# Performance work log

Measured on AMD Instinct MI355X. Metric: run time of the kernel, lower is better.

## Reference

```python
import jax, jax.numpy as jnp
import numpy as np

D_MODEL = 1024
NUM_HEADS = 16
HEAD_DIM = D_MODEL // NUM_HEADS  # used only for score scaling, as in the torch code


def setup_inputs() -> dict:
    key = jax.random.key(0)
    ks = jax.random.split(key, 8)
    B, S, D = 4, 2048, D_MODEL
    w_scale = 1.0 / np.sqrt(D)
    return {
        "x": jax.random.normal(ks[0], (B, S, D), dtype=jnp.float32),
        "Wq": jax.random.normal(ks[1], (D, D), dtype=jnp.float32) * w_scale,
        "bq": jnp.zeros((D,), dtype=jnp.float32),
        "Wk": jax.random.normal(ks[2], (D, D), dtype=jnp.float32) * w_scale,
        "bk": jnp.zeros((D,), dtype=jnp.float32),
        "Wv": jax.random.normal(ks[3], (D, D), dtype=jnp.float32) * w_scale,
        "bv": jnp.zeros((D,), dtype=jnp.float32),
        "temperature_scale": jnp.ones((1,), dtype=jnp.float32),
    }


def reference(x, Wq, bq, Wk, bk, Wv, bv, temperature_scale):
    # q, k, v: (B, S, D) -- no head split in the original module
    q = x @ Wq + bq
    k = x @ Wk + bk
    v = x @ Wv + bv
    scale = jnp.asarray(HEAD_DIM, x.dtype) ** 0.5
    # scores: (B, S, S)
    scores = jnp.einsum("bqd,bkd->bqk", q, k) / scale / temperature_scale[0]
    probs = jax.nn.softmax(scores, axis=-1)
    # per-row attention entropy (B, S, 1)
    entropy = -jnp.sum(probs * jnp.log(probs + 1e-8), axis=-1, keepdims=True)
    attention_output = jnp.einsum("bqk,bkd->bqd", probs, v)
    return attention_output, entropy.mean()
```

## Files before the change

kernel.cpp:

```cpp
#include <hip/hip_runtime.h>
#include <hip/hip_bf16.h>
#include <cstdint>
#include <cstddef>


typedef __attribute__((ext_vector_type(8))) short short8;
typedef __attribute__((ext_vector_type(4))) short short4v;
typedef __attribute__((ext_vector_type(4))) float f32x4;

#define GLOBAL_AS __attribute__((address_space(1)))
#define LDS_AS __attribute__((address_space(3)))

__device__ __forceinline__ void async_load16(const void* g, void* lds) {
  __builtin_amdgcn_global_load_lds((GLOBAL_AS void*)g, (LDS_AS void*)lds, 16, 0, 0);
}

__device__ __forceinline__ short f2bf_s(float x) {
  __hip_bfloat16 h = __float2bfloat16(x);
  return *reinterpret_cast<short*>(&h);
}

template <int MODE>
__device__ __forceinline__
void gemm256_body(const __hip_bfloat16* __restrict__ A,
                  const __hip_bfloat16* __restrict__ Bt,
                  void* __restrict__ Cout,
                  const float* __restrict__ bias,
                  int K, int lda, int ldb, int ldc,
                  __hip_bfloat16* __restrict__ sA,
                  __hip_bfloat16* __restrict__ sB,
                  int m0, int n0,
                  const float* __restrict__ aux,
                  float* __restrict__ stats) {
  const int tid  = threadIdx.x;
  const int lane = tid & 63;
  const int wid  = tid >> 6;
  const int wm   = (wid >> 2) * 128;
  const int wn   = (wid & 3) * 64;
  const int quad = lane >> 4;
  const int rc   = lane & 15;
  const int rc7  = rc & 7;
  const int wnr  = wn & 64;

  f32x4 acc[8][4] = {};

  const int r0   = tid >> 3;
  const int scol = ((tid & 7) ^ (r0 & 7)) * 8;
  const __hip_bfloat16* Ag = A  + (size_t)(m0 + r0) * lda + scol;
  const __hip_bfloat16* Bg = Bt + (size_t)(n0 + r0) * ldb + scol;

  const int NT = K >> 6;

  auto stA = [&](int buf, int half, int kofs) {
    const __hip_bfloat16* s = Ag + (size_t)(half * 128) * lda + kofs;
    __hip_bfloat16* d = sA + (size_t)buf * 16384 + (size_t)half * 8192 + tid * 8;
    async_load16(s, d);
    async_load16(s + (size_t)64 * lda, d + 4096);
  };
  auto stB = [&](int buf, int half, int kofs) {
    const __hip_bfloat16* s = Bg + (size_t)(half * 128) * ldb + kofs;
    __hip_bfloat16* d = sB + (size_t)buf * 16384 + (size_t)half * 8192 + tid * 8;
    async_load16(s, d);
    async_load16(s + (size_t)64 * ldb, d + 4096);
  };

  const __hip_bfloat16* sAh0 = sA + (size_t)(wm >> 7) * 8192;
  const __hip_bfloat16* sBh0 = sB + (size_t)(wn >> 7) * 8192;

  {
    const int k1 = (NT > 1 ? 1 : 0) * 64;
    stA(0, 0, 0); stA(0, 1, 0); stB(0, 0, 0); stB(0, 1, 0);
    stB(1, 0, k1); stB(1, 1, k1); stA(1, 0, k1);
  }
  asm volatile("s_waitcnt vmcnt(6)" ::: "memory");
  __builtin_amdgcn_s_barrier();

  for (int t = 0; t < NT; ++t) {
    const int buf = t & 1;
    const __hip_bfloat16* sAc = sAh0 + buf * 16384;
    const __hip_bfloat16* sBc = sBh0 + buf * 16384;
    const int k1 = ((t + 1 < NT) ? t + 1 : NT - 1) * 64;
    const int k2 = ((t + 2 < NT) ? t + 2 : NT - 1) * 64;

    short8 af[2][4], bfr[2][4], ah[2][4];

#pragma unroll
    for (int kk = 0; kk < 2; ++kk) {
      const int gs = (kk * 4 + quad) ^ rc7;
#pragma unroll
      for (int i = 0; i < 4; ++i)
        af[kk][i] = *(const short8*)&sAc[(i * 16 + rc) * 64 + gs * 8];
#pragma unroll
      for (int j = 0; j < 4; ++j)
        bfr[kk][j] = *(const short8*)&sBc[(wnr + j * 16 + rc) * 64 + gs * 8];
    }
    stA(buf ^ 1, 1, k1);
    __builtin_amdgcn_s_barrier();
    __builtin_amdgcn_s_setprio(1);
#pragma unroll
    for (int mi = 0; mi < 4; ++mi)
#pragma unroll
      for (int ni = 0; ni < 2; ++ni)
#pragma unroll
        for (int kk = 0; kk < 2; ++kk)
          acc[mi][ni] = __builtin_amdgcn_mfma_f32_16x16x32_bf16(
              af[kk][mi], bfr[kk][ni], acc[mi][ni], 0, 0, 0);
    __builtin_amdgcn_s_setprio(0);
    __builtin_amdgcn_s_barrier();

    __builtin_amdgcn_s_setprio(1);
#pragma unroll
    for (int mi = 0; mi < 4; ++mi)
#pragma unroll
      for (int ni = 2; ni < 4; ++ni)
#pragma unroll
        for (int kk = 0; kk < 2; ++kk)
          acc[mi][ni] = __builtin_amdgcn_mfma_f32_16x16x32_bf16(
              af[kk][mi], bfr[kk][ni], acc[mi][ni], 0, 0, 0);
    __builtin_amdgcn_s_setprio(0);
    __builtin_amdgcn_s_barrier();

#pragma unroll
    for (int kk = 0; kk < 2; ++kk) {
      const int gs = (kk * 4 + quad) ^ rc7;
#pragma unroll
      for (int i = 0; i < 4; ++i)
        ah[kk][i] = *(const short8*)&sAc[((i + 4) * 16 + rc) * 64 + gs * 8];
    }
    stB(buf, 0, k2);
    __builtin_amdgcn_s_barrier();
    __builtin_amdgcn_s_setprio(1);
#pragma unroll
    for (int mi = 0; mi < 4; ++mi)
#pragma unroll
      for (int ni = 0; ni < 2; ++ni)
#pragma unroll
        for (int kk = 0; kk < 2; ++kk)
          acc[4 + mi][ni] = __builtin_amdgcn_mfma_f32_16x16x32_bf16(
              ah[kk][mi], bfr[kk][ni], acc[4 + mi][ni], 0, 0, 0);
    __builtin_amdgcn_s_setprio(0);
    __builtin_amdgcn_s_barrier();

    stB(buf, 1, k2);
    stA(buf, 0, k2);
    __builtin_amdgcn_s_barrier();
    __builtin_amdgcn_s_setprio(1);
#pragma unroll
    for (int mi = 0; mi < 4; ++mi)
#pragma unroll
      for (int ni = 2; ni < 4; ++ni)
#pragma unroll
        for (int kk = 0; kk < 2; ++kk)
          acc[4 + mi][ni] = __builtin_amdgcn_mfma_f32_16x16x32_bf16(
              ah[kk][mi], bfr[kk][ni], acc[4 + mi][ni], 0, 0, 0);
    __builtin_amdgcn_s_setprio(0);
    asm volatile("s_waitcnt vmcnt(6)" ::: "memory");
    __builtin_amdgcn_s_barrier();
  }
  asm volatile("s_waitcnt vmcnt(0)" ::: "memory");

  if (MODE == 3) {
    const int chunk = (n0 + wn) >> 6;
#pragma unroll
    for (int mi = 0; mi < 8; ++mi) {
      float l_acc[4] = {}, w_acc[4] = {};
#pragma unroll
      for (int ni = 0; ni < 4; ++ni)
#pragma unroll
        for (int r = 0; r < 4; ++r) {
          const float xv = acc[mi][ni][r];
          const float e = __expf(xv);
          acc[mi][ni][r] = e;
          l_acc[r] += e;
          w_acc[r] += e * xv;
        }
#pragma unroll
      for (int r = 0; r < 4; ++r) {
        float l = l_acc[r], w = w_acc[r];
#pragma unroll
        for (int off = 1; off < 16; off <<= 1) {
          l += __shfl_xor(l, off);
          w += __shfl_xor(w, off);
        }
        if (rc == 0) {
          const int row = m0 + wm + mi * 16 + quad * 4 + r;
          *(float2*)&stats[((size_t)row * 32 + chunk) * 2] = make_float2(l, w);
        }
      }
#pragma unroll
      for (int ni = 0; ni < 4; ++ni) {
        const int col = n0 + wn + ni * 16 + rc;
#pragma unroll
        for (int r = 0; r < 4; ++r) {
          const int row = m0 + wm + mi * 16 + quad * 4 + r;
          ((__hip_bfloat16*)Cout)[(size_t)row * ldc + col] =
              __float2bfloat16(acc[mi][ni][r]);
        }
      }
    }
  } else {
    const float qsc = (MODE == 1 && aux) ? 1.0f / (8.0f * aux[0]) : 1.0f;
#pragma unroll
    for (int mi = 0; mi < 8; ++mi) {
#pragma unroll
      for (int ni = 0; ni < 4; ++ni) {
        const int col = n0 + wn + ni * 16 + rc;
        const float badd = bias[col];
        if (MODE == 2) {
          const int rowb = m0 + wm + mi * 16 + quad * 4;
          short4v o;
#pragma unroll
          for (int r = 0; r < 4; ++r) o[r] = f2bf_s(acc[mi][ni][r] + badd);
          const size_t idx = (size_t)(rowb >> 11) * (1024u * 2048u) +
                             (size_t)col * 2048u + (size_t)(rowb & 2047);
          *(short4v*)((short*)Cout + idx) = o;
        } else {
#pragma unroll
          for (int r = 0; r < 4; ++r) {
            const int row = m0 + wm + mi * 16 + quad * 4 + r;
            ((__hip_bfloat16*)Cout)[(size_t)row * ldc + col] =
                __float2bfloat16((acc[mi][ni][r] + badd) * qsc);
          }
        }
      }
    }
  }
}

__global__ __launch_bounds__(512, 2)
void qkv_fused256(const __hip_bfloat16* __restrict__ xb,
                  const __hip_bfloat16* __restrict__ Wt,
                  __hip_bfloat16* __restrict__ qb, __hip_bfloat16* __restrict__ kb,
                  __hip_bfloat16* __restrict__ vt,
                  const float* __restrict__ bq, const float* __restrict__ bk,
                  const float* __restrict__ bv, const float* __restrict__ tptr) {
  extern __shared__ __align__(16) __hip_bfloat16 smem[];
  __hip_bfloat16* sA = smem;
  __hip_bfloat16* sB = smem + 32768;
  const int lin = blockIdx.x;
  const int G  = (lin & 7) * 48 + (lin >> 3);
  const int mt = G / 12, nt = G % 12;
  const int m0  = mt * 256;
  const int n0g = nt * 256;
  const int z   = n0g >> 10;
  const int n0  = n0g & 1023;
  const __hip_bfloat16* B = Wt + (size_t)z * 1024 * 1024;
  if (z == 0)
    gemm256_body<1>(xb, B, qb, bq, 1024, 1024, 1024, 1024, sA, sB, m0, n0, tptr, nullptr);
  else if (z == 1)
    gemm256_body<1>(xb, B, kb, bk, 1024, 1024, 1024, 1024, sA, sB, m0, n0, nullptr, nullptr);
  else
    gemm256_body<2>(xb, B, vt, bv, 1024, 1024, 1024, 0, sA, sB, m0, n0, nullptr, nullptr);
}

__global__ __launch_bounds__(512, 2)
void scores256(const __hip_bfloat16* __restrict__ qb,
               const __hip_bfloat16* __restrict__ kb,
               __hip_bfloat16* __restrict__ Pt,
               float* __restrict__ stats) {
  extern __shared__ __align__(16) __hip_bfloat16 smem[];
  __hip_bfloat16* sA = smem;
  __hip_bfloat16* sB = smem + 32768;
  const int lin = blockIdx.x;
  const int G = (lin & 7) * 32 + (lin >> 3);
  const int z = G >> 6;
  const int r = G & 63;
  const int y = r >> 3, x = r & 7;
  gemm256_body<3>(qb + (size_t)z * 2048 * 1024, kb + (size_t)z * 2048 * 1024,
                  Pt + (size_t)z * 2048 * 2048, nullptr, 1024, 1024, 1024, 2048,
                  sA, sB, y * 256, x * 256, nullptr, stats + (size_t)z * 2048 * 64);
}

template <int MODE>
__device__ __forceinline__
void gemm_body(const __hip_bfloat16* __restrict__ A,
               const __hip_bfloat16* __restrict__ Bt,
               void* __restrict__ Cout,
               const float* __restrict__ bias,
               int K, int lda, int ldb, int ldc,
               __hip_bfloat16* __restrict__ sA,
               __hip_bfloat16* __restrict__ sB,
               int m0, int n0,
               const float* __restrict__ aux,
               float* __restrict__ stats) {
  const int tid  = threadIdx.x;
  const int lane = tid & 63;
  const int wid  = tid >> 6;
  const int wm = (wid >> 1) * 64;
  const int wn = (wid & 1) * 64;
  const int quad = lane >> 4;
  const int rc   = lane & 15;

  f32x4 acc[4][4] = {};

  const int srow = tid >> 3;
  const int scol = ((tid & 7) ^ ((tid >> 3) & 7)) * 8;
  const __hip_bfloat16* Ag = A  + (size_t)(m0 + srow) * lda + scol;
  const __hip_bfloat16* Bg = Bt + (size_t)(n0 + srow) * ldb + scol;

  for (int k0 = 0; k0 < K; k0 += 64) {
#pragma unroll
    for (int p = 0; p < 4; ++p) {
      async_load16(Ag + k0 + (size_t)(32 * p) * lda, &sA[(wid * 64 + 256 * p) * 8]);
      async_load16(Bg + k0 + (size_t)(32 * p) * ldb, &sB[(wid * 64 + 256 * p) * 8]);
    }
    __syncthreads();

#pragma unroll
    for (int kk = 0; kk < 2; ++kk) {
      const int xo = ((kk * 4 + quad) ^ (rc & 7)) * 8;
      short8 af[4], bf[4];
#pragma unroll
      for (int i = 0; i < 4; ++i)
        af[i] = *(const short8*)&sA[(wm + i * 16 + rc) * 64 + xo];
#pragma unroll
      for (int i = 0; i < 4; ++i)
        bf[i] = *(const short8*)&sB[(wn + i * 16 + rc) * 64 + xo];

#pragma unroll
      for (int mi = 0; mi < 4; ++mi)
#pragma unroll
        for (int ni = 0; ni < 4; ++ni)
          acc[mi][ni] = __builtin_amdgcn_mfma_f32_16x16x32_bf16(
              af[mi], bf[ni], acc[mi][ni], 0, 0, 0);
    }
    __syncthreads();
  }

  if (MODE == 4) {
#pragma unroll
    for (int mi = 0; mi < 4; ++mi) {
      float sc[4];
#pragma unroll
      for (int r = 0; r < 4; ++r)
        sc[r] = aux[m0 + wm + mi * 16 + quad * 4 + r];
#pragma unroll
      for (int ni = 0; ni < 4; ++ni) {
        const int col = n0 + wn + ni * 16 + rc;
#pragma unroll
        for (int r = 0; r < 4; ++r) {
          const int row = m0 + wm + mi * 16 + quad * 4 + r;
          ((float*)Cout)[(size_t)row * ldc + col] = acc[mi][ni][r] * sc[r];
        }
      }
    }
  }
}

__global__ __launch_bounds__(256)
void pv_swz(const __hip_bfloat16* __restrict__ Pt,
            const __hip_bfloat16* __restrict__ vt,
            float* __restrict__ out,
            const float* __restrict__ inv_l) {
  __shared__ __align__(16) __hip_bfloat16 sA[128 * 64];
  __shared__ __align__(16) __hip_bfloat16 sB[128 * 64];
  const int lin = blockIdx.x;
  const int j = lin & 7, t = lin >> 3;
  const int w = t & 3;
  const int G = j + 8 * (t >> 2);
  const size_t z = G >> 5;
  const int r = G & 31;
  const int y = (r >> 2) * 2 + (w >> 1);
  const int x = (r & 3) * 2 + (w & 1);
  gemm_body<4>(Pt + z * 2048 * 2048, vt + z * 1024 * 2048,
               out + z * 2048 * 1024, nullptr, 2048, 2048, 2048, 1024,
               sA, sB, y * 128, x * 128, inv_l + z * 2048, nullptr);
}

__global__ __launch_bounds__(256)
void cast_f32_to_bf16(const float* __restrict__ src,
                      __hip_bfloat16* __restrict__ dst, int n) {
  const int i = (blockIdx.x * 256 + threadIdx.x) * 8;
  if (i >= n) return;
  const float4 a = *(const float4*)(src + i);
  const float4 b = *(const float4*)(src + i + 4);
  short8 o;
  o[0] = f2bf_s(a.x); o[1] = f2bf_s(a.y); o[2] = f2bf_s(a.z); o[3] = f2bf_s(a.w);
  o[4] = f2bf_s(b.x); o[5] = f2bf_s(b.y); o[6] = f2bf_s(b.z); o[7] = f2bf_s(b.w);
  *(short8*)((short*)dst + i) = o;
}

__global__ __launch_bounds__(256)
void transpose_cast_3w(const float* __restrict__ Wq, const float* __restrict__ Wk,
                       const float* __restrict__ Wv,
                       __hip_bfloat16* __restrict__ Wt) {
  __shared__ float tile[64][65];
  const int z = blockIdx.z;
  const float* src = (z == 0) ? Wq : (z == 1) ? Wk : Wv;
  __hip_bfloat16* dst = Wt + (size_t)z * 1024 * 1024;
  const int c0 = blockIdx.x * 64;
  const int r0 = blockIdx.y * 64;
  const int lane = threadIdx.x & 63;
  const int grp  = threadIdx.x >> 6;
#pragma unroll
  for (int i = 0; i < 16; ++i) {
    const int r = grp * 16 + i;
    tile[r][lane] = src[(size_t)(r0 + r) * 1024 + c0 + lane];
  }
  __syncthreads();
#pragma unroll
  for (int i = 0; i < 16; ++i) {
    const int r = grp * 16 + i;
    dst[(size_t)(c0 + r) * 1024 + r0 + lane] = __float2bfloat16(tile[lane][r]);
  }
}

__global__ __launch_bounds__(256)
void stats_reduce(const float* __restrict__ stats,
                  float* __restrict__ inv_l, float* __restrict__ Hrow) {
  const int row = blockIdx.x * 256 + threadIdx.x;
  const float* sp = stats + (size_t)row * 64;
  float l = 0.f, w = 0.f;
#pragma unroll
  for (int j = 0; j < 16; ++j) {
    const float4 a = *(const float4*)(sp + j * 4);
    l += a.x + a.z;
    w += a.y + a.w;
  }
  const float il = 1.0f / l;
  inv_l[row] = il;
  Hrow[row] = __logf(l) - w * il;
}

__global__ __launch_bounds__(256)
void reduce_entropy(const float* __restrict__ Hrow, float* __restrict__ out) {
  const int tid  = threadIdx.x;
  const int lane = tid & 63;
  const int wid  = tid >> 6;
  float s = 0.f;
#pragma unroll
  for (int j = 0; j < 8; ++j) {
    const float4 a = *(const float4*)(Hrow + j * 1024 + tid * 4);
    s += a.x + a.y + a.z + a.w;
  }
#pragma unroll
  for (int off = 1; off < 64; off <<= 1) s += __shfl_xor(s, off);
  __shared__ float red[4];
  if (lane == 0) red[wid] = s;
  __syncthreads();
  if (tid == 0)
    out[0] = (red[0] + red[1] + red[2] + red[3]) * (1.0f / 8192.0f);
}

extern "C" void kernel_launch(void* const* d_in, const int* in_sizes, int n_in,
                              void* d_out, int out_size, void* d_ws, size_t ws_size,
                              hipStream_t stream) {
  const float* x    = (const float*)d_in[0];
  const float* Wq   = (const float*)d_in[1];
  const float* bq   = (const float*)d_in[2];
  const float* Wk   = (const float*)d_in[3];
  const float* bk   = (const float*)d_in[4];
  const float* Wv   = (const float*)d_in[5];
  const float* bv   = (const float*)d_in[6];
  const float* temp = (const float*)d_in[7];
  float* out = (float*)d_out;
  char* ws = (char*)d_ws;

  __hip_bfloat16* qb    = (__hip_bfloat16*)(ws + 0);
  __hip_bfloat16* kb    = (__hip_bfloat16*)(ws + 16777216);
  __hip_bfloat16* vt    = (__hip_bfloat16*)(ws + 33554432);
  __hip_bfloat16* xb    = (__hip_bfloat16*)(ws + 50331648);
  __hip_bfloat16* Wt    = (__hip_bfloat16*)(ws + 67108864);
  __hip_bfloat16* Pt    = (__hip_bfloat16*)(ws + 73400320);
  float*          stats = (float*)(ws + 106954752);
  float*          inv_l = (float*)(ws + 109051904);
  float*          Hrow  = (float*)(ws + 109084672);

  static bool attr_done = false;
  if (!attr_done) {
    hipFuncSetAttribute((const void*)qkv_fused256,
                        hipFuncAttributeMaxDynamicSharedMemorySize, 131072);
    hipFuncSetAttribute((const void*)scores256,
                        hipFuncAttributeMaxDynamicSharedMemorySize, 131072);
    attr_done = true;
  }

  cast_f32_to_bf16<<<4096, 256, 0, stream>>>(x, xb, 8388608);
  transpose_cast_3w<<<dim3(16, 16, 3), 256, 0, stream>>>(Wq, Wk, Wv, Wt);

  qkv_fused256<<<384, 512, 131072, stream>>>(xb, Wt, qb, kb, vt, bq, bk, bv, temp);

  scores256<<<256, 512, 131072, stream>>>(qb, kb, Pt, stats);
  stats_reduce<<<32, 256, 0, stream>>>(stats, inv_l, Hrow);
  pv_swz<<<512, 256, 0, stream>>>(Pt, vt, out, inv_l);

  reduce_entropy<<<1, 256, 0, stream>>>(Hrow, out + 8388608);
}
```

Measured before the change: 256.3 us.

## Restructure GEMM main loop to prefetch next-tile fragments across phases

```diff
diff --git a/kernel.cpp b/kernel.cpp
--- a/kernel.cpp
+++ b/kernel.cpp
@@ -64,37 +64,44 @@
     async_load16(s + (size_t)64 * ldb, d + 4096);
   };
 
-  const __hip_bfloat16* sAh0 = sA + (size_t)(wm >> 7) * 8192;
-  const __hip_bfloat16* sBh0 = sB + (size_t)(wn >> 7) * 8192;
+  const __hip_bfloat16* sAh = sA + (size_t)(wm >> 7) * 8192;
+  const __hip_bfloat16* sBh = sB + (size_t)(wn >> 7) * 8192;
+
+  short8 af[2][4], ah[2][4], blo[2][2], bhi[2][2];
 
   {
-    const int k1 = (NT > 1 ? 1 : 0) * 64;
-    stA(0, 0, 0); stA(0, 1, 0); stB(0, 0, 0); stB(0, 1, 0);
-    stB(1, 0, k1); stB(1, 1, k1); stA(1, 0, k1);
-  }
-  asm volatile("s_waitcnt vmcnt(6)" ::: "memory");
+    const int k1 = (NT > 1) ? 64 : 0;
+    stA(0, 0, 0);  stA(0, 1, 0);  stB(0, 0, 0);  stB(0, 1, 0);
+    stA(1, 0, k1); stA(1, 1, k1); stB(1, 0, k1); stB(1, 1, k1);
+  }
+  asm volatile("s_waitcnt vmcnt(8)" ::: "memory");
   __builtin_amdgcn_s_barrier();
+#pragma unroll
+  for (int kk = 0; kk < 2; ++kk) {
+    const int gs = ((kk * 4 + quad) ^ rc7) * 8;
+#pragma unroll
+    for (int i = 0; i < 4; ++i)
+      af[kk][i] = *(const short8*)&sAh[(i * 16 + rc) * 64 + gs];
+#pragma unroll
+    for (int j = 0; j < 2; ++j)
+      blo[kk][j] = *(const short8*)&sBh[(wnr + j * 16 + rc) * 64 + gs];
+  }
 
   for (int t = 0; t < NT; ++t) {
     const int buf = t & 1;
-    const __hip_bfloat16* sAc = sAh0 + buf * 16384;
-    const __hip_bfloat16* sBc = sBh0 + buf * 16384;
-    const int k1 = ((t + 1 < NT) ? t + 1 : NT - 1) * 64;
+    const __hip_bfloat16* sAc = sAh + buf * 16384;
+    const __hip_bfloat16* sBc = sBh + buf * 16384;
+    const __hip_bfloat16* sAn = sAh + (buf ^ 1) * 16384;
+    const __hip_bfloat16* sBn = sBh + (buf ^ 1) * 16384;
     const int k2 = ((t + 2 < NT) ? t + 2 : NT - 1) * 64;
 
-    short8 af[2][4], bfr[2][4], ah[2][4];
-
 #pragma unroll
     for (int kk = 0; kk < 2; ++kk) {
-      const int gs = (kk * 4 + quad) ^ rc7;
+      const int gs = ((kk * 4 + quad) ^ rc7) * 8;
 #pragma unroll
       for (int i = 0; i < 4; ++i)
-        af[kk][i] = *(const short8*)&sAc[(i * 16 + rc) * 64 + gs * 8];
-#pragma unroll
-      for (int j = 0; j < 4; ++j)
-        bfr[kk][j] = *(const short8*)&sBc[(wnr + j * 16 + rc) * 64 + gs * 8];
-    }
-    stA(buf ^ 1, 1, k1);
+        ah[kk][i] = *(const short8*)&sAc[((i + 4) * 16 + rc) * 64 + gs];
+    }
     __builtin_amdgcn_s_barrier();
     __builtin_amdgcn_s_setprio(1);
 #pragma unroll
@@ -104,30 +111,18 @@
 #pragma unroll
         for (int kk = 0; kk < 2; ++kk)
           acc[mi][ni] = __builtin_amdgcn_mfma_f32_16x16x32_bf16(
-              af[kk][mi], bfr[kk][ni], acc[mi][ni], 0, 0, 0);
+              af[kk][mi], blo[kk][ni], acc[mi][ni], 0, 0, 0);
     __builtin_amdgcn_s_setprio(0);
     __builtin_amdgcn_s_barrier();
 
-    __builtin_amdgcn_s_setprio(1);
-#pragma unroll
-    for (int mi = 0; mi < 4; ++mi)
-#pragma unroll
-      for (int ni = 2; ni < 4; ++ni)
-#pragma unroll
-        for (int kk = 0; kk < 2; ++kk)
-          acc[mi][ni] = __builtin_amdgcn_mfma_f32_16x16x32_bf16(
-              af[kk][mi], bfr[kk][ni], acc[mi][ni], 0, 0, 0);
-    __builtin_amdgcn_s_setprio(0);
-    __builtin_amdgcn_s_barrier();
-
+    stA(buf, 0, k2);
 #pragma unroll
     for (int kk = 0; kk < 2; ++kk) {
-      const int gs = (kk * 4 + quad) ^ rc7;
-#pragma unroll
-      for (int i = 0; i < 4; ++i)
-        ah[kk][i] = *(const short8*)&sAc[((i + 4) * 16 + rc) * 64 + gs * 8];
-    }
-    stB(buf, 0, k2);
+      const int gs = ((kk * 4 + quad) ^ rc7) * 8;
+#pragma unroll
+      for (int j = 0; j < 2; ++j)
+        bhi[kk][j] = *(const short8*)&sBc[(wnr + (j + 2) * 16 + rc) * 64 + gs];
+    }
     __builtin_amdgcn_s_barrier();
     __builtin_amdgcn_s_setprio(1);
 #pragma unroll
@@ -137,24 +132,52 @@
 #pragma unroll
         for (int kk = 0; kk < 2; ++kk)
           acc[4 + mi][ni] = __builtin_amdgcn_mfma_f32_16x16x32_bf16(
-              ah[kk][mi], bfr[kk][ni], acc[4 + mi][ni], 0, 0, 0);
+              ah[kk][mi], blo[kk][ni], acc[4 + mi][ni], 0, 0, 0);
     __builtin_amdgcn_s_setprio(0);
     __builtin_amdgcn_s_barrier();
 
+    asm volatile("s_waitcnt vmcnt(2)" ::: "memory");
+    stA(buf, 1, k2);
+    stB(buf, 0, k2);
+#pragma unroll
+    for (int kk = 0; kk < 2; ++kk) {
+      const int gs = ((kk * 4 + quad) ^ rc7) * 8;
+#pragma unroll
+      for (int j = 0; j < 2; ++j)
+        blo[kk][j] = *(const short8*)&sBn[(wnr + j * 16 + rc) * 64 + gs];
+    }
+    __builtin_amdgcn_s_barrier();
+    __builtin_amdgcn_s_setprio(1);
+#pragma unroll
+    for (int mi = 0; mi < 4; ++mi)
+#pragma unroll
+      for (int nj = 0; nj < 2; ++nj)
+#pragma unroll
+        for (int kk = 0; kk < 2; ++kk)
+          acc[mi][2 + nj] = __builtin_amdgcn_mfma_f32_16x16x32_bf16(
+              af[kk][mi], bhi[kk][nj], acc[mi][2 + nj], 0, 0, 0);
+    __builtin_amdgcn_s_setprio(0);
+    __builtin_amdgcn_s_barrier();
+
     stB(buf, 1, k2);
-    stA(buf, 0, k2);
+#pragma unroll
+    for (int kk = 0; kk < 2; ++kk) {
+      const int gs = ((kk * 4 + quad) ^ rc7) * 8;
+#pragma unroll
+      for (int i = 0; i < 4; ++i)
+        af[kk][i] = *(const short8*)&sAn[(i * 16 + rc) * 64 + gs];
+    }
     __builtin_amdgcn_s_barrier();
     __builtin_amdgcn_s_setprio(1);
 #pragma unroll
     for (int mi = 0; mi < 4; ++mi)
 #pragma unroll
-      for (int ni = 2; ni < 4; ++ni)
+      for (int nj = 0; nj < 2; ++nj)
 #pragma unroll
         for (int kk = 0; kk < 2; ++kk)
-          acc[4 + mi][ni] = __builtin_amdgcn_mfma_f32_16x16x32_bf16(
-              ah[kk][mi], bfr[kk][ni], acc[4 + mi][ni], 0, 0, 0);
+          acc[4 + mi][2 + nj] = __builtin_amdgcn_mfma_f32_16x16x32_bf16(
+              ah[kk][mi], bhi[kk][nj], acc[4 + mi][2 + nj], 0, 0, 0);
     __builtin_amdgcn_s_setprio(0);
-    asm volatile("s_waitcnt vmcnt(6)" ::: "memory");
     __builtin_amdgcn_s_barrier();
   }
   asm volatile("s_waitcnt vmcnt(0)" ::: "memory");
```

After: 263.6 us. 2.9% more time.
